# Kernel optimization log

Hardware: AMD Instinct MI355X
Metric: run time of the kernel (lower is better)

The kernel has to match this reference:

```python
import jax, jax.numpy as jnp
import numpy as np

D_MODEL = 1024
NUM_HEADS = 16
D_K = D_MODEL // NUM_HEADS
B, S = 4, 2048


def setup_inputs() -> dict:
    key = jax.random.key(0)
    ks = jax.random.split(key, 9)
    scale = 1.0 / np.sqrt(D_MODEL)
    x = jax.random.normal(ks[0], (B, S, D_MODEL), dtype=jnp.float32)
    Wq = jax.random.uniform(ks[1], (D_MODEL, D_MODEL), jnp.float32, -scale, scale)
    bq = jax.random.uniform(ks[2], (D_MODEL,), jnp.float32, -scale, scale)
    Wk = jax.random.uniform(ks[3], (D_MODEL, D_MODEL), jnp.float32, -scale, scale)
    bk = jax.random.uniform(ks[4], (D_MODEL,), jnp.float32, -scale, scale)
    Wv = jax.random.uniform(ks[5], (D_MODEL, D_MODEL), jnp.float32, -scale, scale)
    bv = jax.random.uniform(ks[6], (D_MODEL,), jnp.float32, -scale, scale)
    Wo = jax.random.uniform(ks[7], (D_MODEL, D_MODEL), jnp.float32, -scale, scale)
    bo = jax.random.uniform(ks[8], (D_MODEL,), jnp.float32, -scale, scale)
    return {"x": x, "Wq": Wq, "bq": bq, "Wk": Wk, "bk": bk,
            "Wv": Wv, "bv": bv, "Wo": Wo, "bo": bo}


def reference(x, Wq, bq, Wk, bk, Wv, bv, Wo, bo):
    Bsz, Sl, _ = x.shape
    # Linear: x @ W.T + b (torch nn.Linear convention), then split heads -> (B,H,S,d_k)
    def proj(W, b):
        h = jnp.einsum('bsd,ed->bse', x, W) + b
        return h.reshape(Bsz, Sl, NUM_HEADS, D_K).transpose(0, 2, 1, 3)
    q = proj(Wq, bq)
    k = proj(Wk, bk)
    v = proj(Wv, bv)
    scores = jnp.einsum('bhqd,bhkd->bhqk', q, k) / np.sqrt(D_K)
    causal = jnp.tril(jnp.ones((Sl, Sl), dtype=bool))  # True = keep
    scores = jnp.where(causal[None, None], scores, -jnp.inf)
    attn = jax.nn.softmax(scores, axis=-1)
    out = jnp.einsum('bhqk,bhkd->bhqd', attn, v)
    out = out.transpose(0, 2, 1, 3).reshape(Bsz, Sl, D_MODEL)
    return jnp.einsum('bsd,ed->bse', out, Wo) + bo
```

## Files before the change

### kernel.cpp

```cpp
#include <hip/hip_runtime.h>
#include <hip/hip_bf16.h>

typedef __attribute__((ext_vector_type(8))) short short8;
typedef __attribute__((ext_vector_type(4))) short short4v;
typedef __attribute__((ext_vector_type(4))) float floatx4;
typedef __attribute__((ext_vector_type(2))) unsigned int uint2v;
typedef unsigned short u16;

#define B_SZ 4
#define NH   16
#define SEQ  2048
#define DM   1024
#define DK   64
#define M_ROWS (B_SZ * SEQ)

__device__ __forceinline__ u16 f2bf(float f) {
  unsigned u = __float_as_uint(f);
  u += 0x7fff + ((u >> 16) & 1);
  return (u16)(u >> 16);
}

__device__ __forceinline__ unsigned cvt_pk_bf16(float lo, float hi) {
  unsigned r;
  asm("v_cvt_pk_bf16_f32 %0, %1, %2" : "=v"(r) : "v"(lo), "v"(hi));
  return r;
}

__device__ __forceinline__ void async_copy16(const u16* g, const short* lds) {
  __builtin_amdgcn_global_load_lds(
      (const __attribute__((address_space(1))) void*)g,
      (__attribute__((address_space(3))) void*)lds,
      16, 0, 0);
}

#define BAR() do { __builtin_amdgcn_s_barrier(); asm volatile("" ::: "memory"); } while (0)
#define WAIT_LGKM0() asm volatile("s_waitcnt lgkmcnt(0)" ::: "memory")

__global__ __launch_bounds__(256)
void cvt4_kernel(const float* __restrict__ x,
                 const float* __restrict__ wq, const float* __restrict__ wk,
                 const float* __restrict__ wv,
                 u16* __restrict__ xb, u16* __restrict__ wb)
{
  const int y = blockIdx.y;
  const float* src; u16* dst; int n4;
  if (y == 0)      { src = x;  dst = xb;                 n4 = (M_ROWS * DM) / 4; }
  else if (y == 1) { src = wq; dst = wb;                 n4 = (DM * DM) / 4; }
  else if (y == 2) { src = wk; dst = wb + DM * DM;       n4 = (DM * DM) / 4; }
  else             { src = wv; dst = wb + 2 * DM * DM;   n4 = (DM * DM) / 4; }
  for (int i = blockIdx.x * 256 + threadIdx.x; i < n4; i += gridDim.x * 256) {
    floatx4 v = ((const floatx4*)src)[i];
    short4v s;
#pragma unroll
    for (int e = 0; e < 4; ++e) s[e] = (short)f2bf(v[e]);
    ((short4v*)dst)[i] = s;
  }
}

__global__ __launch_bounds__(256)
void cvt1_kernel(const float* __restrict__ in, u16* __restrict__ out, int n4)
{
  for (int i = blockIdx.x * 256 + threadIdx.x; i < n4; i += gridDim.x * 256) {
    floatx4 v = ((const floatx4*)in)[i];
    short4v s;
#pragma unroll
    for (int e = 0; e < 4; ++e) s[e] = (short)f2bf(v[e]);
    ((short4v*)out)[i] = s;
  }
}

__device__ __forceinline__ void stage_tile_half(
    const u16* __restrict__ src,
    short* dst,
    int wid, int lane)
{
#pragma unroll
  for (int j = 0; j < 2; ++j) {
    const int oct = wid + j * 8;
    const int row = oct * 8 + (lane >> 3);
    const int cu  = (lane & 7) ^ (lane >> 3);
    async_copy16(src + (size_t)row * DM + cu * 8, dst + oct * 512);
  }
}

__device__ __forceinline__ void gemm256_core(
    const u16* __restrict__ A, const u16* __restrict__ B,
    int m0, int n0, floatx4 acc[8][4])
{
  __shared__ short smem[65536];

  const int tid  = threadIdx.x;
  const int wid  = tid >> 6;
  const int lane = tid & 63;
  const int wm   = wid >> 2, wn = wid & 3;
  const int quad = lane >> 4, l16 = lane & 15;
  const int swz  = l16 & 7;

  short* sA_[2] = { smem,         smem + 32768 };
  short* sB_[2] = { smem + 16384, smem + 49152 };

#pragma unroll
  for (int mi = 0; mi < 8; ++mi)
#pragma unroll
    for (int ni = 0; ni < 4; ++ni)
      acc[mi][ni] = floatx4{0.f, 0.f, 0.f, 0.f};

  const u16* Abase = A + (size_t)m0 * DM;
  const u16* Bbase = B + (size_t)n0 * DM;

#pragma unroll
  for (int t = 0; t < 2; ++t) {
    const int kof = t * 64;
    stage_tile_half(Abase + kof,                    sA_[t],        wid, lane);
    stage_tile_half(Abase + (size_t)128 * DM + kof, sA_[t] + 8192, wid, lane);
    stage_tile_half(Bbase + kof,                    sB_[t],        wid, lane);
    stage_tile_half(Bbase + (size_t)128 * DM + kof, sB_[t] + 8192, wid, lane);
  }
  asm volatile("s_waitcnt vmcnt(8)" ::: "memory");
  BAR();

  short8 af[4][2], bf0[2][2], bf1[2][2];

  for (int i = 0; i < 8; ++i) {
    const bool nl = (i < 7);
#pragma unroll
    for (int half = 0; half < 2; ++half) {
      short* cA = sA_[half];
      short* cB = sB_[half];
      const int kof_n = (2 * i + 2 + half) * 64;

#pragma unroll
      for (int mi = 0; mi < 4; ++mi)
#pragma unroll
        for (int kk = 0; kk < 2; ++kk)
          af[mi][kk] = *(const short8*)(cA + (wm * 128 + mi * 16 + l16) * 64
                                           + (((kk * 4 + quad) ^ swz) << 3));
#pragma unroll
      for (int ni = 0; ni < 2; ++ni)
#pragma unroll
        for (int kk = 0; kk < 2; ++kk)
          bf0[ni][kk] = *(const short8*)(cB + (wn * 64 + ni * 16 + l16) * 64
                                            + (((kk * 4 + quad) ^ swz) << 3));
      BAR();
      WAIT_LGKM0();
      __builtin_amdgcn_s_setprio(1);
#pragma unroll
      for (int mi = 0; mi < 4; ++mi)
#pragma unroll
        for (int ni = 0; ni < 2; ++ni)
#pragma unroll
          for (int kk = 0; kk < 2; ++kk)
            acc[mi][ni] = __builtin_amdgcn_mfma_f32_16x16x32_bf16(
                af[mi][kk], bf0[ni][kk], acc[mi][ni], 0, 0, 0);
      __builtin_amdgcn_s_setprio(0);
      BAR();

#pragma unroll
      for (int ni = 0; ni < 2; ++ni)
#pragma unroll
        for (int kk = 0; kk < 2; ++kk)
          bf1[ni][kk] = *(const short8*)(cB + (wn * 64 + (2 + ni) * 16 + l16) * 64
                                            + (((kk * 4 + quad) ^ swz) << 3));
      BAR();
      WAIT_LGKM0();
      __builtin_amdgcn_s_setprio(1);
#pragma unroll
      for (int mi = 0; mi < 4; ++mi)
#pragma unroll
        for (int ni = 0; ni < 2; ++ni)
#pragma unroll
          for (int kk = 0; kk < 2; ++kk)
            acc[mi][2 + ni] = __builtin_amdgcn_mfma_f32_16x16x32_bf16(
                af[mi][kk], bf1[ni][kk], acc[mi][2 + ni], 0, 0, 0);
      __builtin_amdgcn_s_setprio(0);
      BAR();

#pragma unroll
      for (int mi = 0; mi < 4; ++mi)
#pragma unroll
        for (int kk = 0; kk < 2; ++kk)
          af[mi][kk] = *(const short8*)(cA + (wm * 128 + (4 + mi) * 16 + l16) * 64
                                           + (((kk * 4 + quad) ^ swz) << 3));
      if (nl) {
        stage_tile_half(Bbase + kof_n,                    cB,        wid, lane);
        stage_tile_half(Bbase + (size_t)128 * DM + kof_n, cB + 8192, wid, lane);
      }
      BAR();
      WAIT_LGKM0();
      __builtin_amdgcn_s_setprio(1);
#pragma unroll
      for (int mi = 0; mi < 4; ++mi)
#pragma unroll
        for (int ni = 0; ni < 2; ++ni)
#pragma unroll
          for (int kk = 0; kk < 2; ++kk)
            acc[4 + mi][2 + ni] = __builtin_amdgcn_mfma_f32_16x16x32_bf16(
                af[mi][kk], bf1[ni][kk], acc[4 + mi][2 + ni], 0, 0, 0);
      __builtin_amdgcn_s_setprio(0);
      BAR();

      if (nl) {
        stage_tile_half(Abase + kof_n,                    cA,        wid, lane);
        stage_tile_half(Abase + (size_t)128 * DM + kof_n, cA + 8192, wid, lane);
        asm volatile("s_waitcnt vmcnt(8)" ::: "memory");
      } else {
        asm volatile("s_waitcnt vmcnt(0)" ::: "memory");
      }
      BAR();
      __builtin_amdgcn_s_setprio(1);
#pragma unroll
      for (int mi = 0; mi < 4; ++mi)
#pragma unroll
        for (int ni = 0; ni < 2; ++ni)
#pragma unroll
          for (int kk = 0; kk < 2; ++kk)
            acc[4 + mi][ni] = __builtin_amdgcn_mfma_f32_16x16x32_bf16(
                af[mi][kk], bf0[ni][kk], acc[4 + mi][ni], 0, 0, 0);
      __builtin_amdgcn_s_setprio(0);
      BAR();
    }
  }
}

__global__ __launch_bounds__(512, 2)
void qkv256_kernel(const u16* __restrict__ xb, const u16* __restrict__ wb,
                   const float* __restrict__ bq, const float* __restrict__ bk,
                   const float* __restrict__ bv,
                   u16* __restrict__ Qo, u16* __restrict__ Ko, u16* __restrict__ Vto)
{
  const int bx = blockIdx.x;
  const int wg = (bx & 7) * 48 + (bx >> 3);
  const int mat = wg >> 7;
  const int r   = wg & 127;

  int m0, n0;
  const u16 *A, *Bm;
  if (mat < 2) { m0 = (r >> 2) * 256; n0 = (r & 3) * 256; A = xb; Bm = wb + (size_t)mat * DM * DM; }
  else         { m0 = (r & 3) * 256;  n0 = (r >> 2) * 256; A = wb + (size_t)2 * DM * DM; Bm = xb; }

  floatx4 acc[8][4];
  gemm256_core(A, Bm, m0, n0, acc);

  const int tid = threadIdx.x;
  const int wid = tid >> 6, lane = tid & 63;
  const int wm = wid >> 2, wn = wid & 3;
  const int quad = lane >> 4, l16 = lane & 15;

  if (mat < 2) {
    u16* dst = (mat == 0) ? Qo : Ko;
    const float* bias = (mat == 0) ? bq : bk;
#pragma unroll
    for (int ni = 0; ni < 4; ++ni) {
      const int n = n0 + wn * 64 + ni * 16 + l16;
      const float bb = bias[n];
      const int h = n >> 6, d = n & 63;
#pragma unroll
      for (int mi = 0; mi < 8; ++mi)
#pragma unroll
        for (int rr = 0; rr < 4; ++rr) {
          const int m = m0 + wm * 128 + mi * 16 + quad * 4 + rr;
          const int b = m >> 11, s = m & 2047;
          dst[((size_t)(b * NH + h) * SEQ + s) * DK + d] = f2bf(acc[mi][ni][rr] + bb);
        }
    }
  } else {
#pragma unroll
    for (int mi = 0; mi < 8; ++mi)
#pragma unroll
      for (int rr = 0; rr < 4; ++rr) {
        const int m = m0 + wm * 128 + mi * 16 + quad * 4 + rr;
        const float bb = bv[m];
        const int h = m >> 6, d = m & 63;
#pragma unroll
        for (int ni = 0; ni < 4; ++ni) {
          const int n = n0 + wn * 64 + ni * 16 + l16;
          const int b = n >> 11, s = n & 2047;
          Vto[((size_t)(b * NH + h) * DK + d) * SEQ + s] = f2bf(acc[mi][ni][rr] + bb);
        }
      }
  }
}

#define AT_STR 72
__global__ __launch_bounds__(256, 2)
void attn_kernel(const u16* __restrict__ Q, const u16* __restrict__ Kx,
                 const u16* __restrict__ Vt, u16* __restrict__ O)
{
  __shared__ short Ks[64 * 64];
  __shared__ short Vs[64 * 64];
  __shared__ __align__(16) short Ps[4 * 16 * AT_STR];

  const int bh  = blockIdx.x;
  const int qtb = 15 - (int)blockIdx.y;
  const int q0  = qtb * 128;
  const int tid = threadIdx.x;
  const int w = tid >> 6, lane = tid & 63;
  const int quad = lane >> 4, l16 = lane & 15;
  const int r8 = lane >> 3, c8 = lane & 7;

  const u16* Qh = Q  + (size_t)bh * SEQ * DK;
  const u16* Kh = Kx + (size_t)bh * SEQ * DK;
  const u16* Vh = Vt + (size_t)bh * DK * SEQ;

  short8 qf[2][2];
#pragma unroll
  for (int qp = 0; qp < 2; ++qp) {
    const int qrow = q0 + w * 32 + qp * 16 + l16;
#pragma unroll
    for (int h = 0; h < 2; ++h)
      qf[qp][h] = *(const short8*)(Qh + (size_t)qrow * DK + h * 32 + quad * 8);
  }

  short8 vone;
#pragma unroll
  for (int j = 0; j < 8; ++j) vone[j] = (l16 == 0) ? (short)0x3F80 : (short)0;

  floatx4 o[2][4], ls[2];
#pragma unroll
  for (int qp = 0; qp < 2; ++qp) {
    ls[qp] = floatx4{0.f, 0.f, 0.f, 0.f};
#pragma unroll
    for (int dt = 0; dt < 4; ++dt) o[qp][dt] = floatx4{0.f, 0.f, 0.f, 0.f};
  }

  const float SC2 = 0.18033688011f;
  const int ktmax = 2 * qtb + 2;
  short* Pw = Ps + w * 16 * AT_STR;

  for (int kt = 0; kt < ktmax; ++kt) {
    const int k0 = kt * 64;
    __syncthreads();
#pragma unroll
    for (int c = 0; c < 2; ++c) {
      const int row8 = w * 16 + c * 8;
      const int sw   = (c8 ^ r8) * 8;
      async_copy16(Kh + (size_t)(k0 + row8 + r8) * DK + sw, Ks + row8 * 64);
      async_copy16(Vh + (size_t)(row8 + r8) * SEQ + k0 + sw, Vs + row8 * 64);
    }
    __syncthreads();

    short8 kf[4][2], vf[4][2];
#pragma unroll
    for (int nt = 0; nt < 4; ++nt)
#pragma unroll
      for (int h = 0; h < 2; ++h) {
        kf[nt][h] = *(const short8*)(Ks + (nt * 16 + l16) * 64 + (((h * 4 + quad) ^ (l16 & 7)) * 8));
        vf[nt][h] = *(const short8*)(Vs + (nt * 16 + l16) * 64 + (((h * 4 + quad) ^ (l16 & 7)) * 8));
      }

#pragma unroll
    for (int qp = 0; qp < 2; ++qp) {
      const int frag0 = q0 + w * 32 + qp * 16;
      if (k0 <= frag0 + 15) {
        floatx4 sc[4];
#pragma unroll
        for (int nt = 0; nt < 4; ++nt) {
          floatx4 z = floatx4{0.f, 0.f, 0.f, 0.f};
          z = __builtin_amdgcn_mfma_f32_16x16x32_bf16(kf[nt][0], qf[qp][0], z, 0, 0, 0);
          z = __builtin_amdgcn_mfma_f32_16x16x32_bf16(kf[nt][1], qf[qp][1], z, 0, 0, 0);
          sc[nt] = z;
        }
        const bool diag = (k0 + 63 > frag0);
        const int qrow = frag0 + l16;
#pragma unroll
        for (int nt = 0; nt < 4; ++nt)
#pragma unroll
          for (int r = 0; r < 4; ++r) {
            float s = sc[nt][r] * SC2;
            if (diag) {
              const int col = k0 + nt * 16 + quad * 4 + r;
              if (col > qrow) s = -1e30f;
            }
            sc[nt][r] = __builtin_amdgcn_exp2f(s);
          }
#pragma unroll
        for (int nt = 0; nt < 4; ++nt) {
          uint2v wv2;
          wv2[0] = cvt_pk_bf16(sc[nt][0], sc[nt][1]);
          wv2[1] = cvt_pk_bf16(sc[nt][2], sc[nt][3]);
          *(short4v*)(Pw + l16 * AT_STR + nt * 16 + quad * 4) =
              __builtin_bit_cast(short4v, wv2);
        }
        asm volatile("" ::: "memory");
        short8 pf[2];
#pragma unroll
        for (int h = 0; h < 2; ++h)
          pf[h] = *(const short8*)(Pw + l16 * AT_STR + h * 32 + quad * 8);
#pragma unroll
        for (int dt = 0; dt < 4; ++dt) {
          o[qp][dt] = __builtin_amdgcn_mfma_f32_16x16x32_bf16(pf[0], vf[dt][0], o[qp][dt], 0, 0, 0);
          o[qp][dt] = __builtin_amdgcn_mfma_f32_16x16x32_bf16(pf[1], vf[dt][1], o[qp][dt], 0, 0, 0);
        }
        ls[qp] = __builtin_amdgcn_mfma_f32_16x16x32_bf16(pf[0], vone, ls[qp], 0, 0, 0);
        ls[qp] = __builtin_amdgcn_mfma_f32_16x16x32_bf16(pf[1], vone, ls[qp], 0, 0, 0);
      }
    }
  }

  const int b = bh >> 4, h = bh & 15;
#pragma unroll
  for (int qp = 0; qp < 2; ++qp) {
    const int frag0 = q0 + w * 32 + qp * 16;
#pragma unroll
    for (int r = 0; r < 4; ++r) {
      const float lv  = __shfl(ls[qp][r], lane & 48);
      const float inv = 1.0f / fmaxf(lv, 1e-20f);
      const int row   = frag0 + quad * 4 + r;
      const size_t base = ((size_t)b * SEQ + row) * DM + h * DK;
#pragma unroll
      for (int dt = 0; dt < 4; ++dt)
        O[base + dt * 16 + l16] = f2bf(o[qp][dt][r] * inv);
    }
  }
}

__global__ __launch_bounds__(512, 2)
void oproj256_kernel(const u16* __restrict__ A, const u16* __restrict__ Wob,
                     const float* __restrict__ bo, float* __restrict__ out)
{
  const int bx = blockIdx.x;
  const int wg = (bx & 7) * 16 + (bx >> 3);
  const int m0 = (wg >> 2) * 256, n0 = (wg & 3) * 256;

  floatx4 acc[8][4];
  gemm256_core(A, Wob, m0, n0, acc);

  const int tid = threadIdx.x;
  const int wid = tid >> 6, lane = tid & 63;
  const int wm = wid >> 2, wn = wid & 3;
  const int quad = lane >> 4, l16 = lane & 15;

#pragma unroll
  for (int ni = 0; ni < 4; ++ni) {
    const int n = n0 + wn * 64 + ni * 16 + l16;
    const float bb = bo[n];
#pragma unroll
    for (int mi = 0; mi < 8; ++mi)
#pragma unroll
      for (int rr = 0; rr < 4; ++rr) {
        const int m = m0 + wm * 128 + mi * 16 + quad * 4 + rr;
        out[(size_t)m * DM + n] = acc[mi][ni][rr] + bb;
      }
  }
}

extern "C" void kernel_launch(void* const* d_in, const int* in_sizes, int n_in,
                              void* d_out, int out_size, void* d_ws, size_t ws_size,
                              hipStream_t stream)
{
  const float* x  = (const float*)d_in[0];
  const float* Wq = (const float*)d_in[1];
  const float* bq = (const float*)d_in[2];
  const float* Wk = (const float*)d_in[3];
  const float* bk = (const float*)d_in[4];
  const float* Wv = (const float*)d_in[5];
  const float* bv = (const float*)d_in[6];
  const float* Wo = (const float*)d_in[7];
  const float* bo = (const float*)d_in[8];
  float* out = (float*)d_out;

  u16* qws  = (u16*)d_ws;
  u16* kws  = qws  + (size_t)M_ROWS * DM;
  u16* vtws = kws  + (size_t)M_ROWS * DM;
  u16* ows  = vtws + (size_t)M_ROWS * DM;

  u16* xb = (u16*)d_out;
  u16* wb = xb + (size_t)M_ROWS * DM;
  u16* wo_b = qws;

  cvt4_kernel  <<<dim3(1024, 4), 256, 0, stream>>>(x, Wq, Wk, Wv, xb, wb);
  qkv256_kernel<<<dim3(384), 512, 0, stream>>>(xb, wb, bq, bk, bv, qws, kws, vtws);
  attn_kernel  <<<dim3(64, 16), 256, 0, stream>>>(qws, kws, vtws, ows);
  cvt1_kernel  <<<dim3(1024), 256, 0, stream>>>(Wo, wo_b, (DM * DM) / 4);
  oproj256_kernel<<<dim3(128), 512, 0, stream>>>(ows, wo_b, bo, out);
}
```

Baseline: 263.1 us.

## Template GEMM core on M tile and restructure LDS/MFMA schedule

Parameterizes the shared GEMM core by the number of M fragments so the output projection uses 128x256 tiles and launches 256 blocks instead of 128, aiming to occupy more compute units. The inner loop is also reorganized to load all B and A fragments up front and issue MFMAs in larger groups with fewer barriers, relying on compiler-inserted waits instead of explicit lgkmcnt waits. The schedule change also affects the QKV GEMM and may change overlap of loads and compute, and smaller tiles reduce per-block data reuse.

Measured after the change: 264.9 us. No clear change (+0.7%).

```diff
diff --git a/kernel.cpp b/kernel.cpp
--- a/kernel.cpp
+++ b/kernel.cpp
@@ -34,7 +34,6 @@
 }
 
 #define BAR() do { __builtin_amdgcn_s_barrier(); asm volatile("" ::: "memory"); } while (0)
-#define WAIT_LGKM0() asm volatile("s_waitcnt lgkmcnt(0)" ::: "memory")
 
 __global__ __launch_bounds__(256)
 void cvt4_kernel(const float* __restrict__ x,
@@ -83,11 +82,16 @@
   }
 }
 
+template<int MIF>
 __device__ __forceinline__ void gemm256_core(
     const u16* __restrict__ A, const u16* __restrict__ B,
-    int m0, int n0, floatx4 acc[8][4])
-{
-  __shared__ short smem[65536];
+    int m0, int n0, floatx4 (&acc)[MIF][4])
+{
+  constexpr int ASH = MIF * 32 * 64;
+  constexpr int AH  = MIF / 4;
+  constexpr int L   = 2 * (AH + 2);
+
+  __shared__ short smem[2 * (ASH + 16384)];
 
   const int tid  = threadIdx.x;
   const int wid  = tid >> 6;
@@ -96,11 +100,11 @@
   const int quad = lane >> 4, l16 = lane & 15;
   const int swz  = l16 & 7;
 
-  short* sA_[2] = { smem,         smem + 32768 };
-  short* sB_[2] = { smem + 16384, smem + 49152 };
-
-#pragma unroll
-  for (int mi = 0; mi < 8; ++mi)
+  short* sA_[2] = { smem,       smem + ASH + 16384 };
+  short* sB_[2] = { smem + ASH, smem + 2 * ASH + 16384 };
+
+#pragma unroll
+  for (int mi = 0; mi < MIF; ++mi)
 #pragma unroll
     for (int ni = 0; ni < 4; ++ni)
       acc[mi][ni] = floatx4{0.f, 0.f, 0.f, 0.f};
@@ -108,18 +112,26 @@
   const u16* Abase = A + (size_t)m0 * DM;
   const u16* Bbase = B + (size_t)n0 * DM;
 
-#pragma unroll
-  for (int t = 0; t < 2; ++t) {
-    const int kof = t * 64;
-    stage_tile_half(Abase + kof,                    sA_[t],        wid, lane);
-    stage_tile_half(Abase + (size_t)128 * DM + kof, sA_[t] + 8192, wid, lane);
-    stage_tile_half(Bbase + kof,                    sB_[t],        wid, lane);
-    stage_tile_half(Bbase + (size_t)128 * DM + kof, sB_[t] + 8192, wid, lane);
-  }
-  asm volatile("s_waitcnt vmcnt(8)" ::: "memory");
+#define STAGE_TILE(kof, c) do {                                              \
+    _Pragma("unroll")                                                        \
+    for (int u = 0; u < AH; ++u)                                             \
+      stage_tile_half(Abase + (size_t)(u * 128) * DM + (kof),                \
+                      sA_[c] + u * 8192, wid, lane);                         \
+    stage_tile_half(Bbase + (kof),                    sB_[c],        wid, lane); \
+    stage_tile_half(Bbase + (size_t)128 * DM + (kof), sB_[c] + 8192, wid, lane); \
+  } while (0)
+
+#define VMCNT_L() do {                                                       \
+    if constexpr (L == 8) asm volatile("s_waitcnt vmcnt(8)" ::: "memory");   \
+    else                  asm volatile("s_waitcnt vmcnt(6)" ::: "memory");   \
+  } while (0)
+
+  STAGE_TILE(0, 0);
+  STAGE_TILE(64, 1);
+  VMCNT_L();
   BAR();
 
-  short8 af[4][2], bf0[2][2], bf1[2][2];
+  short8 af[MIF][2], bf[4][2];
 
   for (int i = 0; i < 8; ++i) {
     const bool nl = (i < 7);
@@ -130,96 +142,82 @@
       const int kof_n = (2 * i + 2 + half) * 64;
 
 #pragma unroll
-      for (int mi = 0; mi < 4; ++mi)
+      for (int nt = 0; nt < 2; ++nt)
 #pragma unroll
         for (int kk = 0; kk < 2; ++kk)
-          af[mi][kk] = *(const short8*)(cA + (wm * 128 + mi * 16 + l16) * 64
+          bf[nt][kk] = *(const short8*)(cB + (wn * 64 + nt * 16 + l16) * 64
                                            + (((kk * 4 + quad) ^ swz) << 3));
 #pragma unroll
-      for (int ni = 0; ni < 2; ++ni)
+      for (int mi = 0; mi < MIF / 2; ++mi)
 #pragma unroll
         for (int kk = 0; kk < 2; ++kk)
-          bf0[ni][kk] = *(const short8*)(cB + (wn * 64 + ni * 16 + l16) * 64
-                                            + (((kk * 4 + quad) ^ swz) << 3));
+          af[mi][kk] = *(const short8*)(cA + (wm * (MIF * 16) + mi * 16 + l16) * 64
+                                           + (((kk * 4 + quad) ^ swz) << 3));
+#pragma unroll
+      for (int nt = 2; nt < 4; ++nt)
+#pragma unroll
+        for (int kk = 0; kk < 2; ++kk)
+          bf[nt][kk] = *(const short8*)(cB + (wn * 64 + nt * 16 + l16) * 64
+                                           + (((kk * 4 + quad) ^ swz) << 3));
+#pragma unroll
+      for (int mi = MIF / 2; mi < MIF; ++mi)
+#pragma unroll
+        for (int kk = 0; kk < 2; ++kk)
+          af[mi][kk] = *(const short8*)(cA + (wm * (MIF * 16) + mi * 16 + l16) * 64
+                                           + (((kk * 4 + quad) ^ swz) << 3));
+
+      __builtin_amdgcn_s_setprio(1);
+#pragma unroll
+      for (int mi = 0; mi < MIF / 2; ++mi)
+#pragma unroll
+        for (int nt = 0; nt < 2; ++nt)
+#pragma unroll
+          for (int kk = 0; kk < 2; ++kk)
+            acc[mi][nt] = __builtin_amdgcn_mfma_f32_16x16x32_bf16(
+                af[mi][kk], bf[nt][kk], acc[mi][nt], 0, 0, 0);
+#pragma unroll
+      for (int mi = 0; mi < MIF / 2; ++mi)
+#pragma unroll
+        for (int nt = 2; nt < 4; ++nt)
+#pragma unroll
+          for (int kk = 0; kk < 2; ++kk)
+            acc[mi][nt] = __builtin_amdgcn_mfma_f32_16x16x32_bf16(
+                af[mi][kk], bf[nt][kk], acc[mi][nt], 0, 0, 0);
+#pragma unroll
+      for (int mi = MIF / 2; mi < MIF; ++mi)
+#pragma unroll
+        for (int nt = 2; nt < 4; ++nt)
+#pragma unroll
+          for (int kk = 0; kk < 2; ++kk)
+            acc[mi][nt] = __builtin_amdgcn_mfma_f32_16x16x32_bf16(
+                af[mi][kk], bf[nt][kk], acc[mi][nt], 0, 0, 0);
+      __builtin_amdgcn_s_setprio(0);
+
       BAR();
-      WAIT_LGKM0();
-      __builtin_amdgcn_s_setprio(1);
-#pragma unroll
-      for (int mi = 0; mi < 4; ++mi)
-#pragma unroll
-        for (int ni = 0; ni < 2; ++ni)
-#pragma unroll
-          for (int kk = 0; kk < 2; ++kk)
-            acc[mi][ni] = __builtin_amdgcn_mfma_f32_16x16x32_bf16(
-                af[mi][kk], bf0[ni][kk], acc[mi][ni], 0, 0, 0);
-      __builtin_amdgcn_s_setprio(0);
-      BAR();
-
-#pragma unroll
-      for (int ni = 0; ni < 2; ++ni)
-#pragma unroll
-        for (int kk = 0; kk < 2; ++kk)
-          bf1[ni][kk] = *(const short8*)(cB + (wn * 64 + (2 + ni) * 16 + l16) * 64
-                                            + (((kk * 4 + quad) ^ swz) << 3));
-      BAR();
-      WAIT_LGKM0();
-      __builtin_amdgcn_s_setprio(1);
-#pragma unroll
-      for (int mi = 0; mi < 4; ++mi)
-#pragma unroll
-        for (int ni = 0; ni < 2; ++ni)
-#pragma unroll
-          for (int kk = 0; kk < 2; ++kk)
-            acc[mi][2 + ni] = __builtin_amdgcn_mfma_f32_16x16x32_bf16(
-                af[mi][kk], bf1[ni][kk], acc[mi][2 + ni], 0, 0, 0);
-      __builtin_amdgcn_s_setprio(0);
-      BAR();
-
-#pragma unroll
-      for (int mi = 0; mi < 4; ++mi)
-#pragma unroll
-        for (int kk = 0; kk < 2; ++kk)
-          af[mi][kk] = *(const short8*)(cA + (wm * 128 + (4 + mi) * 16 + l16) * 64
-                                           + (((kk * 4 + quad) ^ swz) << 3));
+
       if (nl) {
-        stage_tile_half(Bbase + kof_n,                    cB,        wid, lane);
-        stage_tile_half(Bbase + (size_t)128 * DM + kof_n, cB + 8192, wid, lane);
-      }
-      BAR();
-      WAIT_LGKM0();
-      __builtin_amdgcn_s_setprio(1);
-#pragma unroll
-      for (int mi = 0; mi < 4; ++mi)
-#pragma unroll
-        for (int ni = 0; ni < 2; ++ni)
-#pragma unroll
-          for (int kk = 0; kk < 2; ++kk)
-            acc[4 + mi][2 + ni] = __builtin_amdgcn_mfma_f32_16x16x32_bf16(
-                af[mi][kk], bf1[ni][kk], acc[4 + mi][2 + ni], 0, 0, 0);
-      __builtin_amdgcn_s_setprio(0);
-      BAR();
-
-      if (nl) {
-        stage_tile_half(Abase + kof_n,                    cA,        wid, lane);
-        stage_tile_half(Abase + (size_t)128 * DM + kof_n, cA + 8192, wid, lane);
-        asm volatile("s_waitcnt vmcnt(8)" ::: "memory");
+        STAGE_TILE(kof_n, half);
+        VMCNT_L();
       } else {
         asm volatile("s_waitcnt vmcnt(0)" ::: "memory");
       }
-      BAR();
+
       __builtin_amdgcn_s_setprio(1);
 #pragma unroll
-      for (int mi = 0; mi < 4; ++mi)
-#pragma unroll
-        for (int ni = 0; ni < 2; ++ni)
+      for (int mi = MIF / 2; mi < MIF; ++mi)
+#pragma unroll
+        for (int nt = 0; nt < 2; ++nt)
 #pragma unroll
           for (int kk = 0; kk < 2; ++kk)
-            acc[4 + mi][ni] = __builtin_amdgcn_mfma_f32_16x16x32_bf16(
-                af[mi][kk], bf0[ni][kk], acc[4 + mi][ni], 0, 0, 0);
+            acc[mi][nt] = __builtin_amdgcn_mfma_f32_16x16x32_bf16(
+                af[mi][kk], bf[nt][kk], acc[mi][nt], 0, 0, 0);
       __builtin_amdgcn_s_setprio(0);
+
       BAR();
     }
   }
+#undef STAGE_TILE
+#undef VMCNT_L
 }
 
 __global__ __launch_bounds__(512, 2)
@@ -239,7 +237,7 @@
   else         { m0 = (r & 3) * 256;  n0 = (r >> 2) * 256; A = wb + (size_t)2 * DM * DM; Bm = xb; }
 
   floatx4 acc[8][4];
-  gemm256_core(A, Bm, m0, n0, acc);
+  gemm256_core<8>(A, Bm, m0, n0, acc);
 
   const int tid = threadIdx.x;
   const int wid = tid >> 6, lane = tid & 63;
@@ -419,11 +417,11 @@
                      const float* __restrict__ bo, float* __restrict__ out)
 {
   const int bx = blockIdx.x;
-  const int wg = (bx & 7) * 16 + (bx >> 3);
-  const int m0 = (wg >> 2) * 256, n0 = (wg & 3) * 256;
-
-  floatx4 acc[8][4];
-  gemm256_core(A, Wob, m0, n0, acc);
+  const int wg = (bx & 7) * 32 + (bx >> 3);
+  const int m0 = (wg >> 2) * 128, n0 = (wg & 3) * 256;
+
+  floatx4 acc[4][4];
+  gemm256_core<4>(A, Wob, m0, n0, acc);
 
   const int tid = threadIdx.x;
   const int wid = tid >> 6, lane = tid & 63;
@@ -435,10 +433,10 @@
     const int n = n0 + wn * 64 + ni * 16 + l16;
     const float bb = bo[n];
 #pragma unroll
-    for (int mi = 0; mi < 8; ++mi)
+    for (int mi = 0; mi < 4; ++mi)
 #pragma unroll
       for (int rr = 0; rr < 4; ++rr) {
-        const int m = m0 + wm * 128 + mi * 16 + quad * 4 + rr;
+        const int m = m0 + wm * 64 + mi * 16 + quad * 4 + rr;
         out[(size_t)m * DM + n] = acc[mi][ni][rr] + bb;
       }
   }
@@ -472,5 +470,5 @@
   qkv256_kernel<<<dim3(384), 512, 0, stream>>>(xb, wb, bq, bk, bv, qws, kws, vtws);
   attn_kernel  <<<dim3(64, 16), 256, 0, stream>>>(qws, kws, vtws, ows);
   cvt1_kernel  <<<dim3(1024), 256, 0, stream>>>(Wo, wo_b, (DM * DM) / 4);
-  oproj256_kernel<<<dim3(128), 512, 0, stream>>>(ows, wo_b, bo, out);
-}
+  oproj256_kernel<<<dim3(256), 512, 0, stream>>>(ows, wo_b, bo, out);
+}
```
